# Optimization experiments

Hardware: AMD Instinct MI355X
Metric: run time of the kernel (lower is better)

## Reference

```python
import jax, jax.numpy as jnp
import numpy as np

# Dimensions
T, B = 128, 512
NTOK, NINP, NHID = 512, 512, 600
NB, BS, TOPK = 6, 100, 4          # num_blocks, block_size = nhid//num_blocks, update_topk
H, DK, DV, ATT = 4, 64, 85, 340   # input-attention heads, key dim, value dim (H*DV == attention_out)
H2, DK2, DV2 = 4, 32, 32          # communication (step) attention dims


def setup_inputs() -> dict:
    key = jax.random.key(0)
    ks = jax.random.split(key, 16)
    def rn(k, shape, s=0.05):
        return (jax.random.normal(k, shape) * s).astype(jnp.float32)
    return dict(
        input=jax.random.normal(ks[0], (T, B, NTOK), dtype=jnp.float32),
        h0=jnp.zeros((B, NHID), jnp.float32),
        masks=jnp.ones((T, B, 1), jnp.float32),
        enc_W=rn(ks[1], (NTOK, NINP)), enc_b=jnp.zeros((NINP,), jnp.float32),
        Wq_in=rn(ks[2], (BS, H * DK)), Wk_in=rn(ks[3], (NINP, H * DK)), Wv_in=rn(ks[4], (NINP, H * DV)),
        W_ih=rn(ks[5], (NB, ATT, 3 * BS)), W_hh=rn(ks[6], (NB, BS, 3 * BS)),
        b_ih=jnp.zeros((NB, 3 * BS), jnp.float32), b_hh=jnp.zeros((NB, 3 * BS), jnp.float32),
        Wq_c=rn(ks[7], (BS, H2 * DK2)), Wk_c=rn(ks[8], (BS, H2 * DK2)),
        Wv_c=rn(ks[9], (BS, H2 * DV2)), Wo_c=rn(ks[10], (H2 * DV2, BS)),
        dec_W=rn(ks[11], (NHID, NTOK)), dec_b=jnp.zeros((NTOK,), jnp.float32),
    )


def _rim_scan(emb, masks, h0, Wq_in, Wk_in, Wv_in, W_ih, W_hh, b_ih, b_hh,
              Wq_c, Wk_c, Wv_c, Wo_c):
    inv_sdk = 1.0 / np.sqrt(DK).astype(np.float32)
    inv_sdk2 = 1.0 / np.sqrt(DK2).astype(np.float32)

    def step(h, xm):
        xt, mt = xm                      # [B,NINP], [B,1]
        h = h * mt                       # episode-reset gating
        hb = h.reshape(B, NB, BS)
        # --- input attention over {real input, null} slots ---
        slots = jnp.stack([xt, jnp.zeros_like(xt)], axis=1)          # [B,2,NINP]
        k = (slots @ Wk_in).reshape(B, 2, H, DK)
        v = (slots @ Wv_in).reshape(B, 2, H, DV)
        q = (hb @ Wq_in).reshape(B, NB, H, DK)
        att = jax.nn.softmax(jnp.einsum('bnhd,bshd->bnhs', q, k) * inv_sdk, axis=-1)
        act = 1.0 - att[..., 1].mean(-1)                             # [B,NB] attention to real input
        kth = jax.lax.top_k(act, TOPK)[0][:, -1:]
        mask = (act >= kth).astype(h.dtype)                          # [B,NB] top-k block activation
        inp_use = jnp.einsum('bnhs,bshd->bnhd', att, v).reshape(B, NB, ATT)
        # --- block-diagonal GRU update ---
        gi = jnp.einsum('bnd,nde->bne', inp_use, W_ih) + b_ih
        gh = jnp.einsum('bnd,nde->bne', hb, W_hh) + b_hh
        gi_r, gi_z, gi_n = jnp.split(gi, 3, axis=-1)
        gh_r, gh_z, gh_n = jnp.split(gh, 3, axis=-1)
        r = jax.nn.sigmoid(gi_r + gh_r)
        z = jax.nn.sigmoid(gi_z + gh_z)
        n = jnp.tanh(gi_n + r * gh_n)
        hn = (1.0 - z) * n + z * hb
        # --- step (communication) attention across blocks, residual ---
        qc = (hn @ Wq_c).reshape(B, NB, H2, DK2)
        kc = (hn @ Wk_c).reshape(B, NB, H2, DK2)
        vc = (hn @ Wv_c).reshape(B, NB, H2, DV2)
        ac = jax.nn.softmax(jnp.einsum('bnhd,bmhd->bhnm', qc, kc) * inv_sdk2, axis=-1)
        co = jnp.einsum('bhnm,bmhd->bnhd', ac, vc).reshape(B, NB, H2 * DV2) @ Wo_c
        hc = hn + co
        # --- only top-k active blocks are updated ---
        m = mask[..., None]
        hf = (m * hc + (1.0 - m) * hb).reshape(B, NHID)
        return hf, (hf, mask)

    h_last, (hs, bmask) = jax.lax.scan(step, h0, (emb, masks))
    return hs, h_last, bmask


def reference(input, h0, masks, enc_W, enc_b, Wq_in, Wk_in, Wv_in,
              W_ih, W_hh, b_ih, b_hh, Wq_c, Wk_c, Wv_c, Wo_c, dec_W, dec_b):
    emb = input @ enc_W + enc_b                                      # encoder Linear [T,B,NINP]
    hs, h_last, bmask = _rim_scan(emb, masks, h0, Wq_in, Wk_in, Wv_in,
                                  W_ih, W_hh, b_ih, b_hh, Wq_c, Wk_c, Wv_c, Wo_c)
    dec = hs @ dec_W + dec_b                                         # decoder [T,B,NTOK]
    return dec
```

## Files before the change

### kernel.cpp

```cpp
#include <hip/hip_runtime.h>
#include <math.h>

#define T_STEPS 128
#define BATCH   512
#define NTOK    512
#define NINP    512
#define NHID    600
#define NBK     6
#define BS      100
#define HH      4
#define DK      64
#define DV      85
#define ATT     340
#define H2      4
#define DK2     32
#define DV2     32
#define G3      300
#define VN      340
#define KAPN    400
#define CN      740
#define CNP     768
#define UN2     1800
#define UN2P    1920
#define UK0     128
#define KV0     512
#define DECKP   640
#define SW      2

typedef __attribute__((ext_vector_type(8))) short short8;
typedef __attribute__((ext_vector_type(4))) short short4v;
typedef __attribute__((ext_vector_type(4))) float f32x4;

typedef __attribute__((address_space(1))) const unsigned int* g1ptr;
typedef __attribute__((address_space(3))) unsigned int* l3ptr;

__device__ __forceinline__ float sigf(float x) { return 1.f / (1.f + expf(-x)); }
__device__ __forceinline__ unsigned short f2b(float f) {
    unsigned u = __float_as_uint(f);
    unsigned r = (u + 0x7fffu + ((u >> 16) & 1u)) >> 16;
    return (unsigned short)r;
}
__device__ __forceinline__ float b2f(unsigned short u) {
    return __uint_as_float(((unsigned)u) << 16);
}
__device__ __forceinline__ void split3(float x, unsigned short& hi,
                                       unsigned short& mid, unsigned short& lo) {
    hi = f2b(x);
    float r1 = x - b2f(hi);
    mid = f2b(r1);
    lo = f2b(r1 - b2f(mid));
}

struct ZOff { int div; long s1; long s2; };
__device__ __forceinline__ long zoff(ZOff z, int bz) {
    return (long)(bz / z.div) * z.s1 + (long)(bz % z.div) * z.s2;
}

__device__ __forceinline__ void stage_tile(const unsigned short* __restrict__ gbase,
                                           long rowStride, int m0, int k0,
                                           unsigned short* lds, int tid)
{
    const int w = tid >> 6;
#pragma unroll
    for (int q = 0; q < 4; q++) {
        int idx = (q << 8) + tid;
        int r = idx >> 3, ce = (idx & 7) << 3;
        const unsigned short* g = gbase + (long)(m0 + r) * rowStride + k0 + ce;
        unsigned short* l = lds + q * 2048 + w * 512;
        __builtin_amdgcn_global_load_lds((g1ptr)(const void*)g, (l3ptr)(void*)l, 16, 0, 0);
    }
}
__device__ __forceinline__ void stage_tile64(const unsigned short* __restrict__ gbase,
                                             long rowStride, int m0, int k0,
                                             unsigned short* lds, int tid)
{
    const int w = tid >> 6;
#pragma unroll
    for (int q = 0; q < 2; q++) {
        int idx = (q << 8) + tid;
        int r = idx >> 3, ce = (idx & 7) << 3;
        const unsigned short* g = gbase + (long)(m0 + r) * rowStride + k0 + ce;
        unsigned short* l = lds + q * 2048 + w * 512;
        __builtin_amdgcn_global_load_lds((g1ptr)(const void*)g, (l3ptr)(void*)l, 16, 0, 0);
    }
}

__global__ __launch_bounds__(256) void gemm6_useg(
    const unsigned short* __restrict__ A, long aZ,
    const unsigned short* __restrict__ B, long bZ,
    float* __restrict__ C, long cZ, int ldc, int Nreal, int K0)
{
    const int bz = blockIdx.z;
    A += (long)bz * aZ;
    B += (long)bz * bZ;
    C += (long)bz * cZ;
    const int LDA = 3 * K0;
    const int m0 = blockIdx.y * 64, n0 = blockIdx.x * 128;
    __shared__ __align__(16) unsigned short As3[3][64 * 64];
    __shared__ __align__(16) unsigned short Bs3[3][128 * 64];
    const int tid = threadIdx.x;
    const int lane = tid & 63;
    const int w = tid >> 6;

    f32x4 acc[4][2];
#pragma unroll
    for (int m = 0; m < 4; m++)
#pragma unroll
        for (int n = 0; n < 2; n++)
#pragma unroll
            for (int v = 0; v < 4; v++) acc[m][n][v] = 0.f;

    const int segA[6] = {0, 0, 1, 0, 2, 1};
    const int segB[6] = {0, 1, 0, 2, 0, 1};
    for (int k0 = 0; k0 < K0; k0 += 64) {
        __syncthreads();
#pragma unroll
        for (int s = 0; s < 3; s++) stage_tile64(A + s * K0, LDA, m0, k0, As3[s], tid);
#pragma unroll
        for (int s = 0; s < 3; s++) stage_tile(B + s * K0, LDA, n0, k0, Bs3[s], tid);
        __syncthreads();
#pragma unroll
        for (int p = 0; p < 6; p++) {
            const unsigned short* Asl = As3[segA[p]];
            const unsigned short* Bsl = Bs3[segB[p]];
#pragma unroll
            for (int kk = 0; kk < 2; kk++) {
                short8 af[4], bfr[2];
#pragma unroll
                for (int m = 0; m < 4; m++)
                    af[m] = *(const short8*)&Asl[(m * 16 + (lane & 15)) * 64 + kk * 32 + (lane >> 4) * 8];
#pragma unroll
                for (int n = 0; n < 2; n++)
                    bfr[n] = *(const short8*)&Bsl[(w * 32 + n * 16 + (lane & 15)) * 64 + kk * 32 + (lane >> 4) * 8];
#pragma unroll
                for (int m = 0; m < 4; m++)
#pragma unroll
                    for (int n = 0; n < 2; n++)
                        acc[m][n] = __builtin_amdgcn_mfma_f32_16x16x32_bf16(af[m], bfr[n], acc[m][n], 0, 0, 0);
            }
        }
    }
#pragma unroll
    for (int m = 0; m < 4; m++) {
        int rbase = m0 + m * 16 + (lane >> 4) * 4;
#pragma unroll
        for (int n = 0; n < 2; n++) {
            int col = n0 + w * 32 + n * 16 + (lane & 15);
            if (col < Nreal) {
#pragma unroll
                for (int v = 0; v < 4; v++)
                    C[(long)(rbase + v) * ldc + col] = acc[m][n][v];
            }
        }
    }
}

__global__ __launch_bounds__(256) void gemm6_kvseg(
    const float* __restrict__ X,
    const unsigned short* __restrict__ B,
    unsigned short* __restrict__ A_U,
    float* __restrict__ Kbuf,
    const float* __restrict__ bias, int MU)
{
    const int m0 = blockIdx.y * 64, n0 = blockIdx.x * 128;
    __shared__ __align__(16) unsigned short As3[3][64 * 64];
    __shared__ __align__(16) unsigned short Bs3[3][128 * 64];
    const int tid = threadIdx.x;
    const int lane = tid & 63;
    const int w = tid >> 6;

    f32x4 acc[4][2];
#pragma unroll
    for (int m = 0; m < 4; m++)
#pragma unroll
        for (int n = 0; n < 2; n++)
#pragma unroll
            for (int v = 0; v < 4; v++) acc[m][n][v] = 0.f;

    const int segA[6] = {0, 0, 1, 0, 2, 1};
    const int segB[6] = {0, 1, 0, 2, 0, 1};
    for (int k0 = 0; k0 < KV0; k0 += 64) {
        f32x4 xv[4];
#pragma unroll
        for (int q = 0; q < 4; q++) {
            int idx = (q << 8) + tid;
            int r = idx >> 4, c4 = (idx & 15) << 2;
            xv[q] = *(const f32x4*)&X[(long)(m0 + r) * KV0 + k0 + c4];
        }
        __syncthreads();
#pragma unroll
        for (int s = 0; s < 3; s++) stage_tile(B + s * KV0, 3 * KV0, n0, k0, Bs3[s], tid);
#pragma unroll
        for (int q = 0; q < 4; q++) {
            int idx = (q << 8) + tid;
            int r = idx >> 4, c4 = (idx & 15) << 2;
            short4v hs, ms, ls;
#pragma unroll
            for (int j = 0; j < 4; j++) {
                unsigned short h, m, l;
                split3(xv[q][j], h, m, l);
                hs[j] = (short)h; ms[j] = (short)m; ls[j] = (short)l;
            }
            *(short4v*)&As3[0][r * 64 + c4] = hs;
            *(short4v*)&As3[1][r * 64 + c4] = ms;
            *(short4v*)&As3[2][r * 64 + c4] = ls;
        }
        __syncthreads();
#pragma unroll
        for (int p = 0; p < 6; p++) {
            const unsigned short* Asl = As3[segA[p]];
            const unsigned short* Bsl = Bs3[segB[p]];
#pragma unroll
            for (int kk = 0; kk < 2; kk++) {
                short8 af[4], bfr[2];
#pragma unroll
                for (int m = 0; m < 4; m++)
                    af[m] = *(const short8*)&Asl[(m * 16 + (lane & 15)) * 64 + kk * 32 + (lane >> 4) * 8];
#pragma unroll
                for (int n = 0; n < 2; n++)
                    bfr[n] = *(const short8*)&Bsl[(w * 32 + n * 16 + (lane & 15)) * 64 + kk * 32 + (lane >> 4) * 8];
#pragma unroll
                for (int m = 0; m < 4; m++)
#pragma unroll
                    for (int n = 0; n < 2; n++)
                        acc[m][n] = __builtin_amdgcn_mfma_f32_16x16x32_bf16(af[m], bfr[n], acc[m][n], 0, 0, 0);
            }
        }
    }
#pragma unroll
    for (int m = 0; m < 4; m++) {
        int rbase = m0 + m * 16 + (lane >> 4) * 4;
#pragma unroll
        for (int n = 0; n < 2; n++) {
            int col = n0 + w * 32 + n * 16 + (lane & 15);
            if (col < CN) {
                float bv = bias[col];
                if (col < VN) {
                    int h = col / DV, kk2 = col - h * DV;
#pragma unroll
                    for (int v = 0; v < 4; v++) {
                        float val = acc[m][n][v] + bv;
                        unsigned short hi, mid, lo;
                        split3(val, hi, mid, lo);
                        long base = ((long)h * MU + (rbase + v)) * (3 * UK0) + kk2;
                        A_U[base] = hi;
                        A_U[base + UK0] = mid;
                        A_U[base + 2 * UK0] = lo;
                    }
                } else {
                    int kc = col - VN;
#pragma unroll
                    for (int v = 0; v < 4; v++)
                        Kbuf[(long)(rbase + v) * KAPN + kc] = acc[m][n][v] + bv;
                }
            }
        }
    }
}

__global__ __launch_bounds__(256) void gemm_mfma64(
    const unsigned short* __restrict__ A,
    const unsigned short* __restrict__ B,
    float* __restrict__ C, int ldc,
    const float* __restrict__ bias, int Kp)
{
    const int m0 = blockIdx.y * 64, n0 = blockIdx.x * 128;
    __shared__ __align__(16) unsigned short As[64 * 64];
    __shared__ __align__(16) unsigned short Bs[128 * 64];
    const int tid = threadIdx.x;
    const int lane = tid & 63;
    const int w = tid >> 6;

    f32x4 acc[4][2];
#pragma unroll
    for (int m = 0; m < 4; m++)
#pragma unroll
        for (int n = 0; n < 2; n++)
#pragma unroll
            for (int v = 0; v < 4; v++) acc[m][n][v] = 0.f;

    for (int k0 = 0; k0 < Kp; k0 += 64) {
        __syncthreads();
        stage_tile64(A, Kp, m0, k0, As, tid);
        stage_tile(B, Kp, n0, k0, Bs, tid);
        __syncthreads();
#pragma unroll
        for (int kk = 0; kk < 2; kk++) {
            short8 af[4], bfr[2];
#pragma unroll
            for (int m = 0; m < 4; m++)
                af[m] = *(const short8*)&As[(m * 16 + (lane & 15)) * 64 + kk * 32 + (lane >> 4) * 8];
#pragma unroll
            for (int n = 0; n < 2; n++)
                bfr[n] = *(const short8*)&Bs[(w * 32 + n * 16 + (lane & 15)) * 64 + kk * 32 + (lane >> 4) * 8];
#pragma unroll
            for (int m = 0; m < 4; m++)
#pragma unroll
                for (int n = 0; n < 2; n++)
                    acc[m][n] = __builtin_amdgcn_mfma_f32_16x16x32_bf16(af[m], bfr[n], acc[m][n], 0, 0, 0);
        }
    }
#pragma unroll
    for (int m = 0; m < 4; m++) {
        int rbase = m0 + m * 16 + (lane >> 4) * 4;
#pragma unroll
        for (int n = 0; n < 2; n++) {
            int col = n0 + w * 32 + n * 16 + (lane & 15);
            float bv = bias ? bias[col] : 0.f;
#pragma unroll
            for (int v = 0; v < 4; v++)
                C[(long)(rbase + v) * ldc + col] = acc[m][n][v] + bv;
        }
    }
}

__global__ __launch_bounds__(256) void sgemm(
    const float* __restrict__ A, ZOff za, int lda,
    const float* __restrict__ B, ZOff zb, int ldb,
    float* __restrict__ C, ZOff zc, int ldc,
    int M, int N, int K)
{
    const int bz = blockIdx.z;
    A += zoff(za, bz);
    B += zoff(zb, bz);
    C += zoff(zc, bz);
    const int m0 = blockIdx.y * 128, n0 = blockIdx.x * 64;
    __shared__ float As[16][132];
    __shared__ float Bs[16][68];
    const int tid = threadIdx.x;
    const int tm = tid >> 4, tn = tid & 15;
    const int ar = tid >> 1, ak = (tid & 1) * 8;
    const int bk = tid >> 4, bn = (tid & 15) * 4;

    float acc[8][4];
#pragma unroll
    for (int i = 0; i < 8; i++)
#pragma unroll
        for (int j = 0; j < 4; j++) acc[i][j] = 0.f;

    for (int k0 = 0; k0 < K; k0 += 16) {
        float av[8], bv[4];
#pragma unroll
        for (int j = 0; j < 8; j++) {
            int gk = k0 + ak + j;
            av[j] = (gk < K) ? A[(long)(m0 + ar) * lda + gk] : 0.f;
        }
#pragma unroll
        for (int j = 0; j < 4; j++) {
            int gk = k0 + bk, gn = n0 + bn + j;
            bv[j] = (gk < K && gn < N) ? B[(long)gk * ldb + gn] : 0.f;
        }
        __syncthreads();
#pragma unroll
        for (int j = 0; j < 8; j++) As[ak + j][ar] = av[j];
#pragma unroll
        for (int j = 0; j < 4; j++) Bs[bk][bn + j] = bv[j];
        __syncthreads();
#pragma unroll
        for (int kk = 0; kk < 16; kk++) {
            float a[8], b[4];
#pragma unroll
            for (int i = 0; i < 8; i++) a[i] = As[kk][tm * 8 + i];
#pragma unroll
            for (int j = 0; j < 4; j++) b[j] = Bs[kk][tn * 4 + j];
#pragma unroll
            for (int i = 0; i < 8; i++)
#pragma unroll
                for (int j = 0; j < 4; j++)
                    acc[i][j] += a[i] * b[j];
        }
    }
#pragma unroll
    for (int i = 0; i < 8; i++) {
        int gm = m0 + tm * 8 + i;
#pragma unroll
        for (int j = 0; j < 4; j++) {
            int gn = n0 + tn * 4 + j;
            if (gn < N) C[(long)gm * ldc + gn] = acc[i][j];
        }
    }
}

__global__ __launch_bounds__(256) void prep_wqt(const float* __restrict__ Wq_in,
                                                float* __restrict__ WqT)
{
    int idx = blockIdx.x * 256 + threadIdx.x;
    if (idx >= HH * DK * BS) return;
    int h = idx / (DK * BS), r = idx - h * DK * BS, d = r / BS, w = r - d * BS;
    WqT[idx] = Wq_in[w * (HH * DK) + h * DK + d];
}

__global__ __launch_bounds__(256) void prep_whh4(const float* __restrict__ W_hh,
                                                 float* __restrict__ Whh4)
{
    int idx = blockIdx.x * 256 + threadIdx.x;
    if (idx >= NBK * BS * G3) return;
    int n = idx / (BS * G3), r = idx - n * (BS * G3);
    int d = r / G3, e = r - d * G3;
    int g = e / BS, w = e - g * BS;
    Whh4[(((long)n * BS + d) * BS + w) * 4 + g] = W_hh[idx];
}

__global__ __launch_bounds__(256) void bias_k(const float* __restrict__ enc_b,
                                              const float* __restrict__ Wk,
                                              float* __restrict__ kbf)
{
    int j = threadIdx.x;
    if (j >= HH * DK) return;
    float acc = 0.f;
    for (int d = 0; d < NINP; d++) acc += enc_b[d] * Wk[d * (HH * DK) + j];
    kbf[j] = acc;
}

__global__ __launch_bounds__(256) void bias_c_kernel(const float* __restrict__ enc_b,
                                                     const float* __restrict__ Wv,
                                                     const float* __restrict__ kbf,
                                                     const float* __restrict__ WqT,
                                                     float* __restrict__ bias_c)
{
    int j = blockIdx.x * 256 + threadIdx.x;
    if (j >= CNP) return;
    float acc = 0.f;
    if (j < VN) {
        for (int d = 0; d < NINP; d++) acc += enc_b[d] * Wv[d * (HH * DV) + j];
    } else if (j < CN) {
        int r = j - VN;
        int h = r / BS, w = r - h * BS;
        for (int d = 0; d < DK; d++)
            acc += kbf[h * DK + d] * WqT[(h * DK + d) * BS + w];
    }
    bias_c[j] = acc;
}

__global__ __launch_bounds__(256) void cvt_dec(const float* __restrict__ dec_W,
                                               unsigned short* __restrict__ dst)
{
    int idx = blockIdx.x * 256 + threadIdx.x;
    if (idx >= NTOK * DECKP) return;
    int n = idx / DECKP, k = idx - n * DECKP;
    dst[idx] = f2b(k < NHID ? dec_W[k * NTOK + n] : 0.f);
}

__global__ __launch_bounds__(256) void cvt_split_ew(const float* __restrict__ EWfull,
                                                    unsigned short* __restrict__ dst)
{
    int idx = blockIdx.x * 256 + threadIdx.x;
    if (idx >= CNP * NTOK) return;
    int n = idx / NTOK, k = idx - n * NTOK;
    float x = (n < CN) ? EWfull[(long)k * CNP + n] : 0.f;
    unsigned short hi, mid, lo;
    split3(x, hi, mid, lo);
    long base = (long)n * (3 * KV0) + k;
    dst[base] = hi;
    dst[base + KV0] = mid;
    dst[base + 2 * KV0] = lo;
}

__global__ __launch_bounds__(256) void cvt_split_bu2(const float* __restrict__ W_ih,
                                                     unsigned short* __restrict__ dst)
{
    int idx = blockIdx.x * 256 + threadIdx.x;
    if (idx >= HH * UN2P * UK0) return;
    int h = idx / (UN2P * UK0), r = idx - h * (UN2P * UK0);
    int j = r / UK0, kk = r - j * UK0;
    float x = 0.f;
    if (kk < DV && j < UN2) {
        int n = j / G3, e = j - n * G3;
        x = W_ih[((long)n * ATT + h * DV + kk) * G3 + e];
    }
    unsigned short hi, mid, lo;
    split3(x, hi, mid, lo);
    long base = ((long)h * UN2P + j) * (3 * UK0) + kk;
    dst[base] = hi;
    dst[base + UK0] = mid;
    dst[base + 2 * UK0] = lo;
}

__global__ __launch_bounds__(1024) void step_fused(
    const float* __restrict__ h_prev,
    const float* __restrict__ masks_t,
    const float* __restrict__ Kbuf,
    const float* __restrict__ U,
    const float* __restrict__ b_ih, const float* __restrict__ b_hh,
    const float* __restrict__ Whh4,
    const float* __restrict__ Wq_c, const float* __restrict__ Wk_c,
    const float* __restrict__ Wv_c, const float* __restrict__ Wo_c,
    float* __restrict__ h_out,
    unsigned short* __restrict__ A_dec,
    int s_step, int MU)
{
    const int b0 = blockIdx.x * SW, tid = threadIdx.x;
    __shared__ __align__(16) float hbT[NHID][SW];
    __shared__ __align__(16) float hnT[NHID][SW];
    __shared__ __align__(16) float kp[SW][KAPN];
    __shared__ __align__(16) float qcb[SW][768], kcb[SW][768], vcb[SW][768];
    __shared__ __align__(16) float coT[NBK * 128][SW];
    __shared__ float part[SW * 96];
    __shared__ float att[SW][24], mk[SW][NBK];
    __shared__ float lg[SW][144];

    const long rowd0 = (long)s_step * BATCH + b0;
    const int n2 = (tid < 600) ? tid / 100 : 0;
    const int w2 = (tid < 600) ? tid - n2 * 100 : 0;

    float uraw[HH][3][SW];
    if (tid < 600) {
#pragma unroll
        for (int h = 0; h < HH; h++) {
            const float* Uh = U + ((long)h * MU + rowd0) * UN2 + n2 * G3;
#pragma unroll
            for (int s = 0; s < SW; s++)
#pragma unroll
                for (int g = 0; g < 3; g++)
                    uraw[h][g][s] = Uh[(long)s * UN2 + g * BS + w2];
        }
    }

    for (int i = tid; i < SW * NHID; i += 1024) {
        int s = i / NHID, j = i - s * NHID;
        hbT[j][s] = h_prev[(long)(b0 + s) * NHID + j] * masks_t[b0 + s];
    }
    for (int i = tid; i < SW * KAPN; i += 1024) {
        int s = i / KAPN, j = i - s * KAPN;
        kp[s][j] = Kbuf[(rowd0 + s) * KAPN + j];
    }
    __syncthreads();
    if (tid < SW * 96) {
        int g = tid >> 2, q = tid & 3;
        int s = g / 24, r = g - s * 24;
        int n = r >> 2, h = r & 3;
        float acc = 0.f;
        int w0 = q * 25;
        for (int w = w0; w < w0 + 25; w++) acc += hbT[n * BS + w][s] * kp[s][h * BS + w];
        part[tid] = acc;
    }
    __syncthreads();
    if (tid < SW * 24) {
        int s = tid / 24, r = tid - s * 24;
        float l = part[tid * 4] + part[tid * 4 + 1] + part[tid * 4 + 2] + part[tid * 4 + 3];
        att[s][r] = sigf(l * 0.125f);
    }
    __syncthreads();
    if (tid < SW) {
        float a[NBK], av[NBK];
        for (int n = 0; n < NBK; n++) {
            av[n] = 0.25f * (att[tid][n * 4] + att[tid][n * 4 + 1] + att[tid][n * 4 + 2] + att[tid][n * 4 + 3]);
            a[n] = av[n];
        }
        for (int i = 0; i < 4; i++) {
            int mx = i;
            for (int j = i + 1; j < NBK; j++) if (a[j] > a[mx]) mx = j;
            float t = a[i]; a[i] = a[mx]; a[mx] = t;
        }
        float kth = a[3];
        for (int n = 0; n < NBK; n++) mk[tid][n] = (av[n] >= kth) ? 1.f : 0.f;
    }

    if (tid < 600) {
        float gi[3][SW], gh[3][SW];
#pragma unroll
        for (int g = 0; g < 3; g++) {
            float bi = b_ih[n2 * G3 + g * BS + w2];
            float bh = b_hh[n2 * G3 + g * BS + w2];
#pragma unroll
            for (int s = 0; s < SW; s++) { gi[g][s] = bi; gh[g][s] = bh; }
        }
#pragma unroll
        for (int h = 0; h < HH; h++)
#pragma unroll
            for (int s = 0; s < SW; s++) {
                float a = att[s][n2 * 4 + h];
#pragma unroll
                for (int g = 0; g < 3; g++)
                    gi[g][s] += a * uraw[h][g][s];
            }
        const f32x4* Wn4 = ((const f32x4*)Whh4) + (long)n2 * BS * BS + w2;
#pragma unroll 10
        for (int d = 0; d < BS; d++) {
            f32x4 wv = Wn4[(long)d * BS];
            float2 hv = *(const float2*)&hbT[n2 * BS + d][0];
            gh[0][0] += wv[0] * hv.x; gh[0][1] += wv[0] * hv.y;
            gh[1][0] += wv[1] * hv.x; gh[1][1] += wv[1] * hv.y;
            gh[2][0] += wv[2] * hv.x; gh[2][1] += wv[2] * hv.y;
        }
        float2 hnv;
        {
            float rr0 = sigf(gi[0][0] + gh[0][0]);
            float zz0 = sigf(gi[1][0] + gh[1][0]);
            float ng0 = tanhf(gi[2][0] + rr0 * gh[2][0]);
            hnv.x = (1.f - zz0) * ng0 + zz0 * hbT[n2 * BS + w2][0];
            float rr1 = sigf(gi[0][1] + gh[0][1]);
            float zz1 = sigf(gi[1][1] + gh[1][1]);
            float ng1 = tanhf(gi[2][1] + rr1 * gh[2][1]);
            hnv.y = (1.f - zz1) * ng1 + zz1 * hbT[n2 * BS + w2][1];
        }
        *(float2*)&hnT[n2 * BS + w2][0] = hnv;
    }
    __syncthreads();

    if (tid < 768) {
        const int mat = tid >> 8, r = tid & 255, ng = r >> 7, c = r & 127;
        const float* W = (mat == 0) ? Wq_c : ((mat == 1) ? Wk_c : Wv_c);
        float acc[3][SW];
#pragma unroll
        for (int j = 0; j < 3; j++)
#pragma unroll
            for (int s = 0; s < SW; s++) acc[j][s] = 0.f;
#pragma unroll 10
        for (int d = 0; d < BS; d++) {
            float wv = W[d * 128 + c];
#pragma unroll
            for (int j = 0; j < 3; j++) {
                float2 hv = *(const float2*)&hnT[(ng * 3 + j) * BS + d][0];
                acc[j][0] += wv * hv.x;
                acc[j][1] += wv * hv.y;
            }
        }
        float (*dst)[768] = (mat == 0) ? qcb : ((mat == 1) ? kcb : vcb);
#pragma unroll
        for (int j = 0; j < 3; j++)
#pragma unroll
            for (int s = 0; s < SW; s++)
                dst[s][(ng * 3 + j) * 128 + c] = acc[j][s];
    }
    __syncthreads();

    if (tid < SW * 144) {
        int s = tid / 144, r = tid - s * 144;
        int h = r / 36, r2 = r - h * 36, n = r2 / NBK, m = r2 - n * NBK;
        float sv = 0.f;
#pragma unroll
        for (int e4 = 0; e4 < 8; e4++) {
            f32x4 qv = *(const f32x4*)&qcb[s][n * 128 + h * 32 + e4 * 4];
            f32x4 kv = *(const f32x4*)&kcb[s][m * 128 + h * 32 + e4 * 4];
            sv += qv[0] * kv[0] + qv[1] * kv[1] + qv[2] * kv[2] + qv[3] * kv[3];
        }
        lg[s][r] = sv * 0.17677669529663687f;
    }
    __syncthreads();
    if (tid < SW * 24) {
        int s = tid / 24, r = tid - s * 24;
        float* row = &lg[s][r * NBK];
        float mx = row[0];
        for (int m = 1; m < NBK; m++) mx = fmaxf(mx, row[m]);
        float sv = 0.f;
        for (int m = 0; m < NBK; m++) { row[m] = expf(row[m] - mx); sv += row[m]; }
        float inv = 1.f / sv;
        for (int m = 0; m < NBK; m++) row[m] *= inv;
    }
    __syncthreads();
    for (int idx = tid; idx < SW * 768; idx += 1024) {
        int s = idx / 768, r = idx - s * 768;
        int n = r >> 7, d = r & 127, h = d >> 5;
        float a = 0.f;
#pragma unroll
        for (int m = 0; m < NBK; m++) a += lg[s][h * 36 + n * NBK + m] * vcb[s][m * 128 + d];
        coT[r][s] = a;
    }
    __syncthreads();

    if (tid < 600) {
        float a0 = 0.f, a1 = 0.f;
#pragma unroll 8
        for (int d = 0; d < 128; d++) {
            float wv = Wo_c[d * BS + w2];
            float2 cv = *(const float2*)&coT[n2 * 128 + d][0];
            a0 += wv * cv.x;
            a1 += wv * cv.y;
        }
        float2 res;
        float hc0 = hnT[n2 * BS + w2][0] + a0;
        float hc1 = hnT[n2 * BS + w2][1] + a1;
        res.x = (mk[0][n2] > 0.5f) ? hc0 : hbT[n2 * BS + w2][0];
        res.y = (mk[1][n2] > 0.5f) ? hc1 : hbT[n2 * BS + w2][1];
        *(float2*)&hbT[n2 * BS + w2][0] = res;
    }
    __syncthreads();
    for (int i = tid; i < SW * NHID; i += 1024) {
        int s = i / NHID, j = i - s * NHID;
        h_out[(long)(b0 + s) * NHID + j] = hbT[j][s];
    }
    for (int i = tid; i < SW * DECKP; i += 1024) {
        int s = i / DECKP, col = i - s * DECKP;
        A_dec[(rowd0 + s) * DECKP + col] = f2b(col < NHID ? hbT[col][s] : 0.f);
    }
}

extern "C" void kernel_launch(void* const* d_in, const int* in_sizes, int n_in,
                              void* d_out, int out_size, void* d_ws, size_t ws_size,
                              hipStream_t stream)
{
    const float* input = (const float*)d_in[0];
    const float* h0    = (const float*)d_in[1];
    const float* masks = (const float*)d_in[2];
    const float* enc_W = (const float*)d_in[3];
    const float* enc_b = (const float*)d_in[4];
    const float* Wq_in = (const float*)d_in[5];
    const float* Wk_in = (const float*)d_in[6];
    const float* Wv_in = (const float*)d_in[7];
    const float* W_ih  = (const float*)d_in[8];
    const float* W_hh  = (const float*)d_in[9];
    const float* b_ih  = (const float*)d_in[10];
    const float* b_hh  = (const float*)d_in[11];
    const float* Wq_c  = (const float*)d_in[12];
    const float* Wk_c  = (const float*)d_in[13];
    const float* Wv_c  = (const float*)d_in[14];
    const float* Wo_c  = (const float*)d_in[15];
    const float* dec_W = (const float*)d_in[16];
    const float* dec_b = (const float*)d_in[17];
    float* out = (float*)d_out;

    const size_t AL = 256;
    auto pad = [&](size_t x) { return (x + AL - 1) & ~(AL - 1); };
    size_t fixedB = pad((size_t)NTOK * CNP * 4)
                  + pad((size_t)NTOK * 256 * 4)
                  + pad((size_t)HH * DK * BS * 4)
                  + pad((size_t)256 * 4)
                  + pad((size_t)CNP * 4)
                  + pad((size_t)NBK * BS * BS * 4 * 4)
                  + pad((size_t)CNP * 3 * KV0 * 2)
                  + pad((size_t)HH * UN2P * 3 * UK0 * 2)
                  + pad((size_t)NTOK * DECKP * 2)
                  + 2 * pad((size_t)BATCH * NHID * 4);
    auto perC = [&](int C) {
        size_t MU = (size_t)C * BATCH;
        return pad(MU * KAPN * 4)
             + pad((size_t)HH * MU * 3 * UK0 * 2)
             + pad((size_t)HH * MU * UN2 * 4)
             + pad(MU * DECKP * 2);
    };
    int C = 8;
    while (C > 1 && fixedB + perC(C) > ws_size) C >>= 1;
    const int MU = C * BATCH;
    const int NCH = T_STEPS / C;

    char* p = (char*)d_ws;
    auto alloc = [&](size_t bytes) { char* r = p; p += pad(bytes); return r; };
    float*          EWfull = (float*)alloc((size_t)NTOK * CNP * 4);
    float*          EWk    = (float*)alloc((size_t)NTOK * 256 * 4);
    float*          WqT    = (float*)alloc((size_t)HH * DK * BS * 4);
    float*          kbf    = (float*)alloc((size_t)256 * 4);
    float*          bias_c = (float*)alloc((size_t)CNP * 4);
    float*          Whh4   = (float*)alloc((size_t)NBK * BS * BS * 4 * 4);
    unsigned short* B_vkap = (unsigned short*)alloc((size_t)CNP * 3 * KV0 * 2);
    unsigned short* B_U    = (unsigned short*)alloc((size_t)HH * UN2P * 3 * UK0 * 2);
    unsigned short* B_dec  = (unsigned short*)alloc((size_t)NTOK * DECKP * 2);
    float*          hA     = (float*)alloc((size_t)BATCH * NHID * 4);
    float*          hB     = (float*)alloc((size_t)BATCH * NHID * 4);
    float*          Kbuf   = (float*)alloc((size_t)MU * KAPN * 4);
    unsigned short* A_U    = (unsigned short*)alloc((size_t)HH * MU * 3 * UK0 * 2);
    float*          Ubuf   = (float*)alloc((size_t)HH * MU * UN2 * 4);
    unsigned short* A_dec  = (unsigned short*)alloc((size_t)MU * DECKP * 2);

    dim3 blk(256);
    ZOff z0 = {1, 0, 0};

    sgemm<<<dim3(6, 4, 1), blk, 0, stream>>>(
        enc_W, z0, NINP, Wv_in, z0, HH * DV, EWfull, z0, CNP, NTOK, VN, NINP);
    sgemm<<<dim3(4, 4, 1), blk, 0, stream>>>(
        enc_W, z0, NINP, Wk_in, z0, HH * DK, EWk, z0, 256, NTOK, HH * DK, NINP);
    prep_wqt<<<dim3((HH * DK * BS + 255) / 256), blk, 0, stream>>>(Wq_in, WqT);
    prep_whh4<<<dim3((NBK * BS * G3 + 255) / 256), blk, 0, stream>>>(W_hh, Whh4);
    sgemm<<<dim3(2, 4, HH), blk, 0, stream>>>(
        EWk, ZOff{1, DK, 0}, 256, WqT, ZOff{1, (long)DK * BS, 0}, BS,
        EWfull + VN, ZOff{1, BS, 0}, CNP, NTOK, BS, DK);
    bias_k<<<dim3(1), blk, 0, stream>>>(enc_b, Wk_in, kbf);
    bias_c_kernel<<<dim3(3), blk, 0, stream>>>(enc_b, Wv_in, kbf, WqT, bias_c);
    cvt_split_ew<<<dim3((CNP * NTOK + 255) / 256), blk, 0, stream>>>(EWfull, B_vkap);
    cvt_split_bu2<<<dim3((HH * UN2P * UK0 + 255) / 256), blk, 0, stream>>>(W_ih, B_U);
    cvt_dec<<<dim3((NTOK * DECKP + 255) / 256), blk, 0, stream>>>(dec_W, B_dec);

    const float* hp = h0;
    float* hbufs[2] = { hA, hB };
    int t = 0;
    for (int c = 0; c < NCH; c++) {
        gemm6_kvseg<<<dim3(CNP / 128, MU / 64, 1), blk, 0, stream>>>(
            input + (size_t)c * MU * NTOK, B_vkap, A_U, Kbuf, bias_c, MU);
        gemm6_useg<<<dim3(UN2P / 128, MU / 64, HH), blk, 0, stream>>>(
            A_U, (long)MU * 3 * UK0, B_U, (long)UN2P * 3 * UK0,
            Ubuf, (long)MU * UN2, UN2, UN2, UK0);
        for (int s = 0; s < C; s++, t++) {
            float* hout = hbufs[t & 1];
            step_fused<<<dim3(BATCH / SW), dim3(1024), 0, stream>>>(
                hp, masks + (size_t)t * BATCH, Kbuf, Ubuf, b_ih, b_hh, Whh4,
                Wq_c, Wk_c, Wv_c, Wo_c, hout, A_dec, s, MU);
            hp = hout;
        }
        gemm_mfma64<<<dim3(NTOK / 128, MU / 64, 1), blk, 0, stream>>>(
            A_dec, B_dec, out + (size_t)c * MU * NTOK, NTOK, dec_b, DECKP);
    }
}
```

Measured before the change: 5.419 ms.

## Reassociate weight preprocessing: fold Wk·Wq first, split-K fused encoder GEMM

Weight preprocessing previously ran three serial sgemm launches: enc_W@Wv, enc_W@Wk, then a batched product of that result with WqT. Now Wk_in is first combined with WqT into a small KW matrix. A single split-K GEMM then multiplies enc_W by the concatenated [Wv | KW] with 2 K-halves and a larger 64x64-tile grid, and the partial sums are added inside cvt_split_ew. This cuts one serial launch and improves grid parallelism for a tiny one-time preprocessing phase, at the cost of a larger partial buffer and slightly different rounding order.

```diff
diff --git a/kernel.cpp b/kernel.cpp
--- a/kernel.cpp
+++ b/kernel.cpp
@@ -51,11 +51,6 @@
     lo = f2b(r1 - b2f(mid));
 }
 
-struct ZOff { int div; long s1; long s2; };
-__device__ __forceinline__ long zoff(ZOff z, int bz) {
-    return (long)(bz / z.div) * z.s1 + (long)(bz % z.div) * z.s2;
-}
-
 __device__ __forceinline__ void stage_tile(const unsigned short* __restrict__ gbase,
                                            long rowStride, int m0, int k0,
                                            unsigned short* lds, int tid)
@@ -314,71 +309,82 @@
     }
 }
 
-__global__ __launch_bounds__(256) void sgemm(
-    const float* __restrict__ A, ZOff za, int lda,
-    const float* __restrict__ B, ZOff zb, int ldb,
-    float* __restrict__ C, ZOff zc, int ldc,
-    int M, int N, int K)
-{
-    const int bz = blockIdx.z;
-    A += zoff(za, bz);
-    B += zoff(zb, bz);
-    C += zoff(zc, bz);
-    const int m0 = blockIdx.y * 128, n0 = blockIdx.x * 64;
-    __shared__ float As[16][132];
+__global__ __launch_bounds__(256) void kw_kernel(const float* __restrict__ Wk_in,
+                                                 const float* __restrict__ WqT,
+                                                 float* __restrict__ KW)
+{
+    int idx = blockIdx.x * 256 + threadIdx.x;
+    if (idx >= NTOK * KAPN) return;
+    int k = idx / KAPN, r = idx - k * KAPN;
+    int h = r / BS, w = r - h * BS;
+    float acc = 0.f;
+#pragma unroll 8
+    for (int d = 0; d < DK; d++)
+        acc += Wk_in[k * (HH * DK) + h * DK + d] * WqT[(h * DK + d) * BS + w];
+    KW[idx] = acc;
+}
+
+__global__ __launch_bounds__(256) void gemm_ew(const float* __restrict__ enc_W,
+                                               const float* __restrict__ Wv,
+                                               const float* __restrict__ KW,
+                                               float* __restrict__ P)
+{
+    const int m0 = blockIdx.y * 64, j0 = blockIdx.x * 64, kb = blockIdx.z * 256;
+    float* Pz = P + (long)blockIdx.z * NTOK * CNP;
+    __shared__ float As[16][68];
     __shared__ float Bs[16][68];
     const int tid = threadIdx.x;
     const int tm = tid >> 4, tn = tid & 15;
-    const int ar = tid >> 1, ak = (tid & 1) * 8;
-    const int bk = tid >> 4, bn = (tid & 15) * 4;
-
-    float acc[8][4];
-#pragma unroll
-    for (int i = 0; i < 8; i++)
+
+    float acc[4][4];
+#pragma unroll
+    for (int i = 0; i < 4; i++)
 #pragma unroll
         for (int j = 0; j < 4; j++) acc[i][j] = 0.f;
 
-    for (int k0 = 0; k0 < K; k0 += 16) {
-        float av[8], bv[4];
-#pragma unroll
-        for (int j = 0; j < 8; j++) {
-            int gk = k0 + ak + j;
-            av[j] = (gk < K) ? A[(long)(m0 + ar) * lda + gk] : 0.f;
-        }
-#pragma unroll
-        for (int j = 0; j < 4; j++) {
-            int gk = k0 + bk, gn = n0 + bn + j;
-            bv[j] = (gk < K && gn < N) ? B[(long)gk * ldb + gn] : 0.f;
-        }
-        __syncthreads();
-#pragma unroll
-        for (int j = 0; j < 8; j++) As[ak + j][ar] = av[j];
-#pragma unroll
-        for (int j = 0; j < 4; j++) Bs[bk][bn + j] = bv[j];
+    for (int k0 = 0; k0 < 256; k0 += 16) {
+        float av[4], bv[4];
+#pragma unroll
+        for (int e = 0; e < 4; e++) {
+            int i2 = (e << 8) + tid;
+            int r = i2 >> 4, kk = i2 & 15;
+            av[e] = enc_W[(long)(m0 + r) * NINP + kb + k0 + kk];
+            int j = i2 & 63, kk2 = i2 >> 6;
+            int gj = j0 + j, gk = kb + k0 + kk2;
+            float b;
+            if (gj < VN) b = Wv[gk * (HH * DV) + gj];
+            else if (gj < CN) b = KW[gk * KAPN + (gj - VN)];
+            else b = 0.f;
+            bv[e] = b;
+        }
+        __syncthreads();
+#pragma unroll
+        for (int e = 0; e < 4; e++) {
+            int i2 = (e << 8) + tid;
+            As[i2 & 15][i2 >> 4] = av[e];
+            Bs[i2 >> 6][i2 & 63] = bv[e];
+        }
         __syncthreads();
 #pragma unroll
         for (int kk = 0; kk < 16; kk++) {
-            float a[8], b[4];
-#pragma unroll
-            for (int i = 0; i < 8; i++) a[i] = As[kk][tm * 8 + i];
+            float a[4], b[4];
+#pragma unroll
+            for (int i = 0; i < 4; i++) a[i] = As[kk][tm * 4 + i];
 #pragma unroll
             for (int j = 0; j < 4; j++) b[j] = Bs[kk][tn * 4 + j];
 #pragma unroll
-            for (int i = 0; i < 8; i++)
+            for (int i = 0; i < 4; i++)
 #pragma unroll
                 for (int j = 0; j < 4; j++)
                     acc[i][j] += a[i] * b[j];
         }
-    }
-#pragma unroll
-    for (int i = 0; i < 8; i++) {
-        int gm = m0 + tm * 8 + i;
-#pragma unroll
-        for (int j = 0; j < 4; j++) {
-            int gn = n0 + tn * 4 + j;
-            if (gn < N) C[(long)gm * ldc + gn] = acc[i][j];
-        }
-    }
+        __syncthreads();
+    }
+#pragma unroll
+    for (int i = 0; i < 4; i++)
+#pragma unroll
+        for (int j = 0; j < 4; j++)
+            Pz[(long)(m0 + tm * 4 + i) * CNP + j0 + tn * 4 + j] = acc[i][j];
 }
 
 __global__ __launch_bounds__(256) void prep_wqt(const float* __restrict__ Wq_in,
@@ -441,13 +447,15 @@
     dst[idx] = f2b(k < NHID ? dec_W[k * NTOK + n] : 0.f);
 }
 
-__global__ __launch_bounds__(256) void cvt_split_ew(const float* __restrict__ EWfull,
+__global__ __launch_bounds__(256) void cvt_split_ew(const float* __restrict__ P,
                                                     unsigned short* __restrict__ dst)
 {
     int idx = blockIdx.x * 256 + threadIdx.x;
     if (idx >= CNP * NTOK) return;
     int n = idx / NTOK, k = idx - n * NTOK;
-    float x = (n < CN) ? EWfull[(long)k * CNP + n] : 0.f;
+    float x = 0.f;
+    if (n < CN)
+        x = P[(long)k * CNP + n] + P[(long)NTOK * CNP + (long)k * CNP + n];
     unsigned short hi, mid, lo;
     split3(x, hi, mid, lo);
     long base = (long)n * (3 * KV0) + k;
@@ -712,8 +720,8 @@
 
     const size_t AL = 256;
     auto pad = [&](size_t x) { return (x + AL - 1) & ~(AL - 1); };
-    size_t fixedB = pad((size_t)NTOK * CNP * 4)
-                  + pad((size_t)NTOK * 256 * 4)
+    size_t fixedB = pad((size_t)2 * NTOK * CNP * 4)
+                  + pad((size_t)NTOK * KAPN * 4)
                   + pad((size_t)HH * DK * BS * 4)
                   + pad((size_t)256 * 4)
                   + pad((size_t)CNP * 4)
@@ -736,8 +744,8 @@
 
     char* p = (char*)d_ws;
     auto alloc = [&](size_t bytes) { char* r = p; p += pad(bytes); return r; };
-    float*          EWfull = (float*)alloc((size_t)NTOK * CNP * 4);
-    float*          EWk    = (float*)alloc((size_t)NTOK * 256 * 4);
+    float*          Pbuf   = (float*)alloc((size_t)2 * NTOK * CNP * 4);
+    float*          KW     = (float*)alloc((size_t)NTOK * KAPN * 4);
     float*          WqT    = (float*)alloc((size_t)HH * DK * BS * 4);
     float*          kbf    = (float*)alloc((size_t)256 * 4);
     float*          bias_c = (float*)alloc((size_t)CNP * 4);
@@ -753,20 +761,14 @@
     unsigned short* A_dec  = (unsigned short*)alloc((size_t)MU * DECKP * 2);
 
     dim3 blk(256);
-    ZOff z0 = {1, 0, 0};
-
-    sgemm<<<dim3(6, 4, 1), blk, 0, stream>>>(
-        enc_W, z0, NINP, Wv_in, z0, HH * DV, EWfull, z0, CNP, NTOK, VN, NINP);
-    sgemm<<<dim3(4, 4, 1), blk, 0, stream>>>(
-        enc_W, z0, NINP, Wk_in, z0, HH * DK, EWk, z0, 256, NTOK, HH * DK, NINP);
+
     prep_wqt<<<dim3((HH * DK * BS + 255) / 256), blk, 0, stream>>>(Wq_in, WqT);
     prep_whh4<<<dim3((NBK * BS * G3 + 255) / 256), blk, 0, stream>>>(W_hh, Whh4);
-    sgemm<<<dim3(2, 4, HH), blk, 0, stream>>>(
-        EWk, ZOff{1, DK, 0}, 256, WqT, ZOff{1, (long)DK * BS, 0}, BS,
-        EWfull + VN, ZOff{1, BS, 0}, CNP, NTOK, BS, DK);
+    kw_kernel<<<dim3((NTOK * KAPN + 255) / 256), blk, 0, stream>>>(Wk_in, WqT, KW);
+    gemm_ew<<<dim3(CNP / 64, NTOK / 64, 2), blk, 0, stream>>>(enc_W, Wv_in, KW, Pbuf);
     bias_k<<<dim3(1), blk, 0, stream>>>(enc_b, Wk_in, kbf);
     bias_c_kernel<<<dim3(3), blk, 0, stream>>>(enc_b, Wv_in, kbf, WqT, bias_c);
-    cvt_split_ew<<<dim3((CNP * NTOK + 255) / 256), blk, 0, stream>>>(EWfull, B_vkap);
+    cvt_split_ew<<<dim3((CNP * NTOK + 255) / 256), blk, 0, stream>>>(Pbuf, B_vkap);
     cvt_split_bu2<<<dim3((HH * UN2P * UK0 + 255) / 256), blk, 0, stream>>>(W_ih, B_U);
     cvt_dec<<<dim3((NTOK * DECKP + 255) / 256), blk, 0, stream>>>(dec_W, B_dec);
 
```

Measured after the change: 5.280 ms. -2.6%, faster.
